# Kernel optimization log

Measured on AMD Instinct MI355X. Metric: run time of the kernel, lower is better.

The kernel has to match this reference:

```python
import jax, jax.numpy as jnp
import numpy as np


def setup_inputs() -> dict:
    key = jax.random.key(0)
    ks = jax.random.split(key, 7)
    B, C, L, A = 8, 1024, 2048, 128
    x = jax.random.normal(ks[0], (B, C, L), dtype=jnp.float32)
    Wk = jax.random.normal(ks[1], (A, C), dtype=jnp.float32) * (1.0 / np.sqrt(C))
    bk = jax.random.normal(ks[2], (A,), dtype=jnp.float32) * 0.01
    Wq = jax.random.normal(ks[3], (A, C), dtype=jnp.float32) * (1.0 / np.sqrt(C))
    bq = jax.random.normal(ks[4], (A,), dtype=jnp.float32) * 0.01
    Wp = jax.random.normal(ks[5], (C, C), dtype=jnp.float32) * (1.0 / np.sqrt(C))
    bp = jax.random.normal(ks[6], (C,), dtype=jnp.float32) * 0.01
    return {"x": x, "Wk": Wk, "bk": bk, "Wq": Wq, "bq": bq, "Wp": Wp, "bp": bp}


def reference(x, Wk, bk, Wq, bq, Wp, bp):
    # x: [B, C, L]; 1x1 Conv1d == pointwise linear over channel dim
    keys = jnp.einsum('bcl,ac->bal', x, Wk) + bk[None, :, None]      # [B, A, L]
    queries = jnp.einsum('bcl,ac->bal', x, Wq) + bq[None, :, None]   # [B, A, L]
    values = jnp.einsum('bal,bam->blm', keys, queries)               # keys^T @ queries -> [B, L, L]
    seqlen = x.shape[2]
    # NOTE: source uses seqlen ** 1 / 2 which is seqlen/2 due to Python precedence
    attn = jax.nn.softmax(values / (seqlen / 2.0), axis=-1)          # [B, L, L]
    out = jnp.einsum('bcl,blm->bcm', x, attn)                        # x @ attn -> [B, C, L]
    out = jnp.einsum('bcm,dc->bdm', out, Wp) + bp[None, :, None]     # output projection
    return out
```

## Files before the change

kernel.cpp:

```cpp
#include <hip/hip_runtime.h>
#include <hip/hip_bf16.h>

typedef __hip_bfloat16 bf16;
typedef __attribute__((ext_vector_type(8))) short bfrag8;
typedef __attribute__((ext_vector_type(8))) int intx8;
typedef __attribute__((ext_vector_type(4))) float floatx4;


__device__ __forceinline__ unsigned char f2fp8(float f) {
    f = fminf(fmaxf(f, -448.f), 448.f);
    return (unsigned char)(__builtin_amdgcn_cvt_pk_fp8_f32(f, f, 0, false) & 0xFF);
}

__device__ __forceinline__ void async_copy16(const void* g, void* lds) {
    __builtin_amdgcn_global_load_lds(
        (const __attribute__((address_space(1))) unsigned int*)g,
        (__attribute__((address_space(3))) unsigned int*)lds, 16, 0, 0);
}

template<int BIASMODE, int OUTKIND, bool EXPZ, bool MFAST>
__global__ __launch_bounds__(256)
void gemm128(const bf16* __restrict__ Ag, long sAb, int lda,
             const bf16* __restrict__ Bg, long sBb, int ldb,
             void* __restrict__ Cg, long sCb, int ldc,
             const float* __restrict__ scl, const float* __restrict__ b2,
             float* __restrict__ Zp, int K, int logfast)
{
    __shared__ unsigned short As[128 * 64];
    __shared__ unsigned short Bs[128 * 64];

    const int lin = blockIdx.x;
    const int bz  = lin & 7;
    const int s   = lin >> 3;
    const int msk = (1 << logfast) - 1;
    int mT, nT;
    if (MFAST) { mT = s & msk; nT = s >> logfast; }
    else       { nT = s & msk; mT = s >> logfast; }

    const bf16* A  = Ag + (size_t)bz * sAb + (size_t)mT * 128 * lda;
    const bf16* Bp = Bg + (size_t)bz * sBb + (size_t)nT * 128 * ldb;
    const int t = threadIdx.x, wave = t >> 6, lane = t & 63;
    const int qrow = lane & 15, quad = lane >> 4;
    const int wr = (wave >> 1) * 64, wc = (wave & 1) * 64;

    floatx4 acc[4][4] = {};

    for (int k0 = 0; k0 < K; k0 += 64) {
        #pragma unroll
        for (int j = 0; j < 4; ++j) {
            int c = j * 256 + t;
            int r = c >> 3, p = c & 7;
            int g = p ^ (r & 7);
            async_copy16(A + (size_t)r * lda + k0 + g * 8, &As[c * 8]);
        }
        #pragma unroll
        for (int j = 0; j < 4; ++j) {
            int c = j * 256 + t;
            int r = c >> 3, p = c & 7;
            int g = p ^ (r & 7);
            async_copy16(Bp + (size_t)r * ldb + k0 + g * 8, &Bs[c * 8]);
        }
        __syncthreads();

        #pragma unroll
        for (int ks = 0; ks < 2; ++ks) {
            bfrag8 af[4], bfv[4];
            #pragma unroll
            for (int mi = 0; mi < 4; ++mi) {
                int row = wr + mi * 16 + qrow;
                int ck  = ks * 4 + quad;
                af[mi] = *(const bfrag8*)&As[row * 64 + ((ck ^ (row & 7)) * 8)];
            }
            #pragma unroll
            for (int ni = 0; ni < 4; ++ni) {
                int row = wc + ni * 16 + qrow;
                int ck  = ks * 4 + quad;
                bfv[ni] = *(const bfrag8*)&Bs[row * 64 + ((ck ^ (row & 7)) * 8)];
            }
            #pragma unroll
            for (int mi = 0; mi < 4; ++mi)
                #pragma unroll
                for (int ni = 0; ni < 4; ++ni)
                    acc[mi][ni] = __builtin_amdgcn_mfma_f32_16x16x32_bf16(
                        af[mi], bfv[ni], acc[mi][ni], 0, 0, 0);
        }
        __syncthreads();
    }

    const int bmr = mT * 128 + wr, bnc = nT * 128 + wc;
    float zp[4] = {0.f, 0.f, 0.f, 0.f};
    #pragma unroll
    for (int mi = 0; mi < 4; ++mi) {
        #pragma unroll
        for (int ni = 0; ni < 4; ++ni) {
            int col = bnc + ni * 16 + qrow;
            #pragma unroll
            for (int r = 0; r < 4; ++r) {
                int row = bmr + mi * 16 + quad * 4 + r;
                float v = acc[mi][ni][r];
                if (EXPZ) { float e = __expf(v); zp[ni] += e; v = (e - 1.0f) * 4096.0f; }
                if (BIASMODE == 1) v = v * scl[col] + b2[col];
                if (BIASMODE == 2) v += scl[row];
                if (OUTKIND == 1)
                    ((float*)Cg + (size_t)bz * sCb)[(size_t)row * ldc + col] = v;
                else if (OUTKIND == 0)
                    ((bf16*)Cg + (size_t)bz * sCb)[(size_t)row * ldc + col] = __float2bfloat16(v);
                else
                    ((unsigned char*)Cg + (size_t)bz * sCb)[(size_t)row * ldc + col] = f2fp8(v);
            }
        }
    }
    if (EXPZ) {
        #pragma unroll
        for (int ni = 0; ni < 4; ++ni) {
            float tt = zp[ni];
            tt += __shfl_xor(tt, 16, 64);
            tt += __shfl_xor(tt, 32, 64);
            if (quad == 0)
                atomicAdd(&Zp[bz * 2048 + bnc + ni * 16 + qrow], tt);
        }
    }
}

__global__ __launch_bounds__(512, 2)
void gemm_s3(const bf16* __restrict__ Ag, long sAb, int lda,
             const bf16* __restrict__ Bg, long sBb, int ldb,
             unsigned char* __restrict__ Cg, long sCb, int ldc,
             float* __restrict__ Zp)
{
    __shared__ __align__(16) unsigned char smem[131072];

    const int lin = blockIdx.x;
    const int bz  = lin & 7;
    const int s0  = lin >> 3;
    const int nT  = s0 & 7, mT = s0 >> 3;

    const bf16* A  = Ag + (size_t)bz * sAb + (size_t)mT * 256 * lda;
    const bf16* Bp = Bg + (size_t)bz * sBb + (size_t)nT * 256 * ldb;
    const int t = threadIdx.x, wave = t >> 6, lane = t & 63;
    const int qrow = lane & 15, quad = lane >> 4;
    const int wm = (wave >> 2) * 128;
    const int wn = (wave & 3) * 64;

    unsigned char* As = smem;
    unsigned char* Bs = smem + 65536;

    #pragma unroll
    for (int j = 0; j < 8; ++j) {
        int c = j * 512 + t;
        int r = c >> 4, p = c & 15;
        int g = (p & 8) | ((p & 7) ^ (r & 7));
        async_copy16(A + (size_t)r * lda + g * 8, As + c * 16);
    }
    #pragma unroll
    for (int j = 0; j < 8; ++j) {
        int c = j * 512 + t;
        int r = c >> 4, p = c & 15;
        int g = (p & 8) | ((p & 7) ^ (r & 7));
        async_copy16(Bp + (size_t)r * ldb + g * 8, Bs + c * 16);
    }
    asm volatile("s_waitcnt vmcnt(0)" ::: "memory");
    __builtin_amdgcn_s_barrier();

    floatx4 acc[8][4] = {};
    #pragma unroll
    for (int ks = 0; ks < 4; ++ks) {
        const int ck = ks * 4 + quad;
        bfrag8 bfv[4];
        #pragma unroll
        for (int ni = 0; ni < 4; ++ni) {
            int row = wn + ni * 16 + qrow;
            int ph  = (ck & 8) | ((ck & 7) ^ (row & 7));
            bfv[ni] = *(const bfrag8*)&Bs[row * 256 + ph * 16];
        }
        #pragma unroll
        for (int mi = 0; mi < 8; ++mi) {
            int row = wm + mi * 16 + qrow;
            int ph  = (ck & 8) | ((ck & 7) ^ (row & 7));
            bfrag8 af = *(const bfrag8*)&As[row * 256 + ph * 16];
            #pragma unroll
            for (int ni = 0; ni < 4; ++ni)
                acc[mi][ni] = __builtin_amdgcn_mfma_f32_16x16x32_bf16(
                    af, bfv[ni], acc[mi][ni], 0, 0, 0);
        }
    }

    const int bmr = mT * 256 + wm, bnc = nT * 256 + wn;
    unsigned char* C8 = Cg + (size_t)bz * sCb;
    float zp[4] = {0.f, 0.f, 0.f, 0.f};
    #pragma unroll
    for (int mi = 0; mi < 8; ++mi) {
        #pragma unroll
        for (int ni = 0; ni < 4; ++ni) {
            int col = bnc + ni * 16 + qrow;
            #pragma unroll
            for (int r = 0; r < 4; ++r) {
                int row = bmr + mi * 16 + quad * 4 + r;
                float e = __expf(acc[mi][ni][r]);
                zp[ni] += e;
                C8[(size_t)row * ldc + col] = f2fp8((e - 1.0f) * 4096.0f);
            }
        }
    }
    #pragma unroll
    for (int ni = 0; ni < 4; ++ni) {
        float tt = zp[ni];
        tt += __shfl_xor(tt, 16, 64);
        tt += __shfl_xor(tt, 32, 64);
        if (quad == 0)
            atomicAdd(&Zp[bz * 2048 + bnc + ni * 16 + qrow], tt);
    }
}

template<int MODE, bool MFAST>
__global__ __launch_bounds__(512, 2)
void gemm_f8(const unsigned char* __restrict__ Ag, long sAb, int lda,
             const unsigned char* __restrict__ Bg, long sBb, int ldb,
             void* __restrict__ Cg, long sCb, int ldc,
             const float* __restrict__ rowb, float os, int K, int logfast)
{
    __shared__ __align__(16) unsigned char smem[131072];

    const int lin = blockIdx.x;
    const int bz  = lin & 7;
    const int s0  = lin >> 3;
    const int msk = (1 << logfast) - 1;
    int mT, nT;
    if (MFAST) { mT = s0 & msk; nT = s0 >> logfast; }
    else       { nT = s0 & msk; mT = s0 >> logfast; }

    const unsigned char* A  = Ag + (size_t)bz * sAb + (size_t)mT * 256 * lda;
    const unsigned char* Bp = Bg + (size_t)bz * sBb + (size_t)nT * 256 * ldb;
    const int t = threadIdx.x, wave = t >> 6, lane = t & 63;
    const int qrow = lane & 15, quad = lane >> 4;
    const int wm = (wave >> 2) * 128;
    const int wn = (wave & 3) * 64;

    floatx4 acc[8][4] = {};

    auto stage_part = [&](int kt, int slot, int part) {
        const int k0 = kt << 7;
        unsigned char* Ad = &smem[slot * 32768];
        unsigned char* Bd = &smem[65536 + slot * 32768];
        #pragma unroll
        for (int j = 0; j < 2; ++j) {
            int c = (part * 2 + j) * 512 + t;
            int r = c >> 3, p = c & 7, g = p ^ (r & 7);
            async_copy16(A + (size_t)r * lda + k0 + g * 16, Ad + c * 16);
        }
        #pragma unroll
        for (int j = 0; j < 2; ++j) {
            int c = (part * 2 + j) * 512 + t;
            int r = c >> 3, p = c & 7, g = p ^ (r & 7);
            async_copy16(Bp + (size_t)r * ldb + k0 + g * 16, Bd + c * 16);
        }
    };

    const int NT = K >> 7;
    stage_part(0, 0, 0);
    stage_part(0, 0, 1);

    for (int kt = 0; kt < NT; ++kt) {
        const int slot = kt & 1;
        const unsigned char* As = &smem[slot * 32768];
        const unsigned char* Bs = &smem[65536 + slot * 32768];

        asm volatile("s_waitcnt vmcnt(0)" ::: "memory");
        __builtin_amdgcn_sched_barrier(0);
        __builtin_amdgcn_s_barrier();
        __builtin_amdgcn_sched_barrier(0);

        intx8 bfr[4];
        #pragma unroll
        for (int ph = 0; ph < 4; ++ph) {
            if (ph == 0) {
                #pragma unroll
                for (int ni = 0; ni < 4; ++ni) {
                    int row = wn + ni * 16 + qrow, sw = row & 7;
                    union { intx8 v; uint4 q[2]; } u;
                    u.q[0] = *(const uint4*)&Bs[row * 128 + (((quad * 2    ) ^ sw) * 16)];
                    u.q[1] = *(const uint4*)&Bs[row * 128 + (((quad * 2 + 1) ^ sw) * 16)];
                    bfr[ni] = u.v;
                }
            }
            intx8 af0, af1;
            {
                int row = wm + (2 * ph) * 16 + qrow, sw = row & 7;
                union { intx8 v; uint4 q[2]; } u;
                u.q[0] = *(const uint4*)&As[row * 128 + (((quad * 2    ) ^ sw) * 16)];
                u.q[1] = *(const uint4*)&As[row * 128 + (((quad * 2 + 1) ^ sw) * 16)];
                af0 = u.v;
            }
            {
                int row = wm + (2 * ph + 1) * 16 + qrow, sw = row & 7;
                union { intx8 v; uint4 q[2]; } u;
                u.q[0] = *(const uint4*)&As[row * 128 + (((quad * 2    ) ^ sw) * 16)];
                u.q[1] = *(const uint4*)&As[row * 128 + (((quad * 2 + 1) ^ sw) * 16)];
                af1 = u.v;
            }
            if (ph < 2 && kt + 1 < NT) stage_part(kt + 1, slot ^ 1, ph);

            __builtin_amdgcn_sched_barrier(0);
            __builtin_amdgcn_s_barrier();
            asm volatile("s_waitcnt lgkmcnt(0)" ::: "memory");
            __builtin_amdgcn_sched_barrier(0);

            __builtin_amdgcn_s_setprio(1);
            #pragma unroll
            for (int ni = 0; ni < 4; ++ni)
                acc[2 * ph][ni] = __builtin_amdgcn_mfma_scale_f32_16x16x128_f8f6f4(
                    af0, bfr[ni], acc[2 * ph][ni], 0, 0, 0, 127, 0, 127);
            #pragma unroll
            for (int ni = 0; ni < 4; ++ni)
                acc[2 * ph + 1][ni] = __builtin_amdgcn_mfma_scale_f32_16x16x128_f8f6f4(
                    af1, bfr[ni], acc[2 * ph + 1][ni], 0, 0, 0, 127, 0, 127);
            __builtin_amdgcn_s_setprio(0);

            __builtin_amdgcn_sched_barrier(0);
            __builtin_amdgcn_s_barrier();
            __builtin_amdgcn_sched_barrier(0);
        }
    }

    const int bmr = mT * 256 + wm, bnc = nT * 256 + wn;
    #pragma unroll
    for (int mi = 0; mi < 8; ++mi) {
        int row0 = bmr + mi * 16 + quad * 4;
        float4 rb4;
        if (MODE == 2) rb4 = *(const float4*)&rowb[bz * 1024 + row0];
        #pragma unroll
        for (int ni = 0; ni < 4; ++ni) {
            int col = bnc + ni * 16 + qrow;
            floatx4 a = acc[mi][ni];
            if (MODE == 2) {
                float* Co = (float*)Cg + (size_t)bz * sCb;
                Co[(size_t)(row0 + 0) * ldc + col] = a[0] * os + rb4.x;
                Co[(size_t)(row0 + 1) * ldc + col] = a[1] * os + rb4.y;
                Co[(size_t)(row0 + 2) * ldc + col] = a[2] * os + rb4.z;
                Co[(size_t)(row0 + 3) * ldc + col] = a[3] * os + rb4.w;
            } else {
                unsigned char* C8 = (unsigned char*)Cg + (size_t)bz * sCb;
                #pragma unroll
                for (int r = 0; r < 4; ++r)
                    C8[(size_t)(row0 + r) * ldc + col] = f2fp8(a[r] * os);
            }
        }
    }
}

__global__ __launch_bounds__(256)
void conv_w(const float* __restrict__ Wk, const float* __restrict__ Wq,
            const float* __restrict__ Wp, bf16* __restrict__ Wkqb,
            unsigned char* __restrict__ Wp8)
{
    int i = blockIdx.x * 256 + threadIdx.x;
    if (i < 32768) {
        const float* src = (i < 16384) ? Wk : Wq;
        int off = (i < 16384) ? i : i - 16384;
        bf16* dst = Wkqb + (size_t)((i < 16384) ? 0 : 131072);
        const float4* sp = (const float4*)src + (size_t)off * 2;
        float4 a = sp[0], b = sp[1];
        union { uint4 u; unsigned short h[8]; } o;
        union { bf16 h; unsigned short u; } cv;
        cv.h = __float2bfloat16(a.x); o.h[0] = cv.u;
        cv.h = __float2bfloat16(a.y); o.h[1] = cv.u;
        cv.h = __float2bfloat16(a.z); o.h[2] = cv.u;
        cv.h = __float2bfloat16(a.w); o.h[3] = cv.u;
        cv.h = __float2bfloat16(b.x); o.h[4] = cv.u;
        cv.h = __float2bfloat16(b.y); o.h[5] = cv.u;
        cv.h = __float2bfloat16(b.z); o.h[6] = cv.u;
        cv.h = __float2bfloat16(b.w); o.h[7] = cv.u;
        ((uint4*)dst)[off] = o.u;
    } else {
        int off = i - 32768;
        const float4* sp = (const float4*)Wp + (size_t)off * 2;
        float4 a = sp[0], b = sp[1];
        unsigned char o[8];
        o[0] = f2fp8(a.x * 2048.f); o[1] = f2fp8(a.y * 2048.f);
        o[2] = f2fp8(a.z * 2048.f); o[3] = f2fp8(a.w * 2048.f);
        o[4] = f2fp8(b.x * 2048.f); o[5] = f2fp8(b.y * 2048.f);
        o[6] = f2fp8(b.z * 2048.f); o[7] = f2fp8(b.w * 2048.f);
        uint2 w;
        w.x = (unsigned int)o[0] | ((unsigned int)o[1] << 8) | ((unsigned int)o[2] << 16) | ((unsigned int)o[3] << 24);
        w.y = (unsigned int)o[4] | ((unsigned int)o[5] << 8) | ((unsigned int)o[6] << 16) | ((unsigned int)o[7] << 24);
        ((uint2*)Wp8)[off] = w;
    }
}

__global__ __launch_bounds__(256)
void conv_x(const float* __restrict__ x, bf16* __restrict__ xt)
{
    const int b = blockIdx.z;
    const int l0 = blockIdx.x * 64, c0 = blockIdx.y * 64;
    const float* xp = x + (size_t)b * 1024 * 2048;
    bf16* xtp = xt + (size_t)b * 2048 * 1024;
    __shared__ unsigned short tile[64][65];
    const int t = threadIdx.x, tr = t >> 4, tc4 = (t & 15) * 4;
    union { bf16 h; unsigned short u; } cv;
    #pragma unroll
    for (int i = 0; i < 4; ++i) {
        int r = i * 16 + tr;
        float4 v = *(const float4*)(xp + (size_t)(c0 + r) * 2048 + l0 + tc4);
        cv.h = __float2bfloat16(v.x); tile[r][tc4]     = cv.u;
        cv.h = __float2bfloat16(v.y); tile[r][tc4 + 1] = cv.u;
        cv.h = __float2bfloat16(v.z); tile[r][tc4 + 2] = cv.u;
        cv.h = __float2bfloat16(v.w); tile[r][tc4 + 3] = cv.u;
    }
    __syncthreads();
    #pragma unroll
    for (int i = 0; i < 4; ++i) {
        int lr = i * 16 + tr;
        union { uint2 u; unsigned short h[4]; } o;
        #pragma unroll
        for (int j = 0; j < 4; ++j) o.h[j] = tile[tc4 + j][lr];
        *(uint2*)(xtp + (size_t)(l0 + lr) * 1024 + c0 + tc4) = o.u;
    }
}

__global__ void prep_bias(const float* __restrict__ bk, const float* __restrict__ bq,
                          float* __restrict__ scl, float* __restrict__ b2, float kscale)
{
    int t = threadIdx.x;
    float s = (t < 128) ? kscale : 1.0f;
    scl[t] = s;
    b2[t] = ((t < 128) ? bk[t] : bq[t - 128]) * s;
}

__global__ __launch_bounds__(256)
void normx(const float* __restrict__ x, const float* __restrict__ Z,
           unsigned char* __restrict__ xs, float* __restrict__ colsum)
{
    const int bc = blockIdx.x;
    const int b  = bc >> 10;
    const int t  = threadIdx.x;
    const float* xp = x + (size_t)bc * 2048 + t * 8;
    const float* zp = Z + b * 2048 + t * 8;
    float4 a = ((const float4*)xp)[0], c4 = ((const float4*)xp)[1];
    float4 z0 = ((const float4*)zp)[0], z1 = ((const float4*)zp)[1];
    float v[8];
    v[0] = a.x  / fmaxf(z0.x, 1e-10f); v[1] = a.y / fmaxf(z0.y, 1e-10f);
    v[2] = a.z  / fmaxf(z0.z, 1e-10f); v[3] = a.w / fmaxf(z0.w, 1e-10f);
    v[4] = c4.x / fmaxf(z1.x, 1e-10f); v[5] = c4.y / fmaxf(z1.y, 1e-10f);
    v[6] = c4.z / fmaxf(z1.z, 1e-10f); v[7] = c4.w / fmaxf(z1.w, 1e-10f);
    float s = 0.f;
    unsigned char o[8];
    #pragma unroll
    for (int j = 0; j < 8; ++j) { s += v[j]; o[j] = f2fp8(v[j] * 65536.f); }
    uint2 w;
    w.x = (unsigned int)o[0] | ((unsigned int)o[1] << 8) | ((unsigned int)o[2] << 16) | ((unsigned int)o[3] << 24);
    w.y = (unsigned int)o[4] | ((unsigned int)o[5] << 8) | ((unsigned int)o[6] << 16) | ((unsigned int)o[7] << 24);
    ((uint2*)(xs + (size_t)bc * 2048))[t] = w;
    #pragma unroll
    for (int off = 32; off >= 1; off >>= 1) s += __shfl_xor(s, off, 64);
    __shared__ float red[4];
    if ((t & 63) == 0) red[t >> 6] = s;
    __syncthreads();
    if (t == 0) colsum[bc] = red[0] + red[1] + red[2] + red[3];
}

__global__ __launch_bounds__(256)
void basek(const float* __restrict__ Wp, const float* __restrict__ colsum,
           const float* __restrict__ bp, float* __restrict__ base)
{
    const int d = blockIdx.x, t = threadIdx.x;
    float4 w = *(const float4*)(Wp + (size_t)d * 1024 + t * 4);
    float pb[8];
    #pragma unroll
    for (int b = 0; b < 8; ++b) {
        float4 cs = *(const float4*)(colsum + b * 1024 + t * 4);
        pb[b] = w.x * cs.x + w.y * cs.y + w.z * cs.z + w.w * cs.w;
    }
    __shared__ float red[8][4];
    #pragma unroll
    for (int b = 0; b < 8; ++b) {
        float s = pb[b];
        #pragma unroll
        for (int off = 32; off >= 1; off >>= 1) s += __shfl_xor(s, off, 64);
        if ((t & 63) == 0) red[b][t >> 6] = s;
    }
    __syncthreads();
    if (t < 8) base[t * 1024 + d] = bp[d] + red[t][0] + red[t][1] + red[t][2] + red[t][3];
}

extern "C" void kernel_launch(void* const* d_in, const int* in_sizes, int n_in,
                              void* d_out, int out_size, void* d_ws, size_t ws_size,
                              hipStream_t stream)
{
    const float* x  = (const float*)d_in[0];
    const float* Wk = (const float*)d_in[1];
    const float* bk = (const float*)d_in[2];
    const float* Wq = (const float*)d_in[3];
    const float* bq = (const float*)d_in[4];
    const float* Wp = (const float*)d_in[5];
    const float* bp = (const float*)d_in[6];
    float* out = (float*)d_out;

    const float kscale = 2.0f / 2048.0f;

    bf16* xt   = (bf16*)d_ws;
    bf16* KQt  = xt + (size_t)8 * 2048 * 1024;
    bf16* Wkqb = KQt + (size_t)8 * 2048 * 256;
    unsigned char* Wp8 = (unsigned char*)(Wkqb + (size_t)256 * 1024);
    unsigned char* St8 = Wp8 + (size_t)1048576;
    unsigned char* xs8 = St8 + (size_t)8 * 2048 * 2048;
    float* Z      = (float*)(xs8 + (size_t)8 * 1024 * 2048);
    float* colsum = Z + 8 * 2048;
    float* base   = colsum + 8 * 1024;
    float* scl    = base + 8 * 1024;
    float* b2     = scl + 256;
    unsigned char* Dlt = (unsigned char*)xt;

    dim3 blk(256, 1, 1);
    dim3 blk512(512, 1, 1);

    prep_bias<<<dim3(1), blk, 0, stream>>>(bk, bq, scl, b2, kscale);
    conv_w<<<dim3(640), blk, 0, stream>>>(Wk, Wq, Wp, Wkqb, Wp8);
    conv_x<<<dim3(32, 16, 8), blk, 0, stream>>>(x, xt);

    gemm128<1, 0, false, false><<<dim3(8 * 16 * 2), blk, 0, stream>>>(
        xt, 2048L * 1024, 1024,  Wkqb, 0, 1024,
        KQt, 2048L * 256, 256,  scl, b2, nullptr, 1024, 1);

    hipMemsetAsync(Z, 0, (size_t)8 * 2048 * sizeof(float), stream);

    gemm_s3<<<dim3(8 * 8 * 8), blk512, 0, stream>>>(
        KQt + 128, 2048L * 256, 256,  KQt, 2048L * 256, 256,
        St8, 2048L * 2048, 2048,  Z);

    normx<<<dim3(8 * 1024), blk, 0, stream>>>(x, Z, xs8, colsum);
    basek<<<dim3(1024), blk, 0, stream>>>(Wp, colsum, bp, base);

    gemm_f8<0, false><<<dim3(8 * 8 * 4), blk512, 0, stream>>>(
        St8, 2048L * 2048, 2048,  xs8, 1024L * 2048, 2048,
        Dlt, 2048L * 1024, 1024,  nullptr, 0.0009765625f, 2048, 2);

    gemm_f8<2, true><<<dim3(8 * 4 * 8), blk512, 0, stream>>>(
        Wp8, 0, 1024,  Dlt, 2048L * 1024, 1024,
        out, 1024L * 2048, 2048,  base, 1.862645149230957e-9f, 1024, 2);
}
```

Before: 261.8 us.

## Fuse x transpose/bf16 conversion into K/Q projection GEMM and merge setup kernels

Removes the separate conv_x transpose pass by having the K/Q projection GEMM load fp32 x tiles directly into LDS and convert them to bf16 while building MFMA fragments. It also folds prep_bias and the Z memset into the weight-conversion kernel, which cuts the launch count. The GEMM now uses 64x256 tiles with 256 blocks. Doing the conversion in the inner loop adds strided LDS reads and VALU work, and 256 blocks may underfill the GPU.

Result: faster. 245.4 us (-6.3%).

```diff
diff --git a/kernel.cpp b/kernel.cpp
--- a/kernel.cpp
+++ b/kernel.cpp
@@ -18,106 +18,84 @@
         (__attribute__((address_space(3))) unsigned int*)lds, 16, 0, 0);
 }
 
-template<int BIASMODE, int OUTKIND, bool EXPZ, bool MFAST>
 __global__ __launch_bounds__(256)
-void gemm128(const bf16* __restrict__ Ag, long sAb, int lda,
-             const bf16* __restrict__ Bg, long sBb, int ldb,
-             void* __restrict__ Cg, long sCb, int ldc,
-             const float* __restrict__ scl, const float* __restrict__ b2,
-             float* __restrict__ Zp, int K, int logfast)
-{
-    __shared__ unsigned short As[128 * 64];
-    __shared__ unsigned short Bs[128 * 64];
+void gemm12(const float* __restrict__ xg, const bf16* __restrict__ Wkqb,
+            bf16* __restrict__ KQt, const float* __restrict__ scl,
+            const float* __restrict__ b2)
+{
+    __shared__ __align__(16) float Xs[64 * 64];
+    __shared__ __align__(16) unsigned short Ws[256 * 64];
 
     const int lin = blockIdx.x;
     const int bz  = lin & 7;
-    const int s   = lin >> 3;
-    const int msk = (1 << logfast) - 1;
-    int mT, nT;
-    if (MFAST) { mT = s & msk; nT = s >> logfast; }
-    else       { nT = s & msk; mT = s >> logfast; }
-
-    const bf16* A  = Ag + (size_t)bz * sAb + (size_t)mT * 128 * lda;
-    const bf16* Bp = Bg + (size_t)bz * sBb + (size_t)nT * 128 * ldb;
+    const int mT  = lin >> 3;
+    const int l0  = mT * 64;
+    const float* xp = xg + (size_t)bz * 1024 * 2048;
+
     const int t = threadIdx.x, wave = t >> 6, lane = t & 63;
     const int qrow = lane & 15, quad = lane >> 4;
-    const int wr = (wave >> 1) * 64, wc = (wave & 1) * 64;
-
-    floatx4 acc[4][4] = {};
-
-    for (int k0 = 0; k0 < K; k0 += 64) {
+    const int wr = (wave >> 1) * 32, wc = (wave & 1) * 128;
+
+    floatx4 acc[2][8] = {};
+
+    for (int k0 = 0; k0 < 1024; k0 += 64) {
         #pragma unroll
         for (int j = 0; j < 4; ++j) {
-            int c = j * 256 + t;
-            int r = c >> 3, p = c & 7;
-            int g = p ^ (r & 7);
-            async_copy16(A + (size_t)r * lda + k0 + g * 8, &As[c * 8]);
-        }
-        #pragma unroll
-        for (int j = 0; j < 4; ++j) {
-            int c = j * 256 + t;
-            int r = c >> 3, p = c & 7;
-            int g = p ^ (r & 7);
-            async_copy16(Bp + (size_t)r * ldb + k0 + g * 8, &Bs[c * 8]);
-        }
+            int ci = j * 256 + t;
+            int r = ci >> 4, li = (ci & 15) * 4;
+            async_copy16(xp + (size_t)(k0 + r) * 2048 + l0 + li, &Xs[ci * 4]);
+        }
+        #pragma unroll
+        for (int j = 0; j < 8; ++j) {
+            int ci = j * 256 + t;
+            int r = ci >> 3, p = ci & 7, g = p ^ (r & 7);
+            async_copy16(Wkqb + (size_t)r * 1024 + k0 + g * 8, &Ws[ci * 8]);
+        }
+        asm volatile("s_waitcnt vmcnt(0)" ::: "memory");
         __syncthreads();
 
         #pragma unroll
         for (int ks = 0; ks < 2; ++ks) {
-            bfrag8 af[4], bfv[4];
-            #pragma unroll
-            for (int mi = 0; mi < 4; ++mi) {
-                int row = wr + mi * 16 + qrow;
-                int ck  = ks * 4 + quad;
-                af[mi] = *(const bfrag8*)&As[row * 64 + ((ck ^ (row & 7)) * 8)];
-            }
-            #pragma unroll
-            for (int ni = 0; ni < 4; ++ni) {
+            const int ck = ks * 4 + quad;
+            bfrag8 bfv[8];
+            #pragma unroll
+            for (int ni = 0; ni < 8; ++ni) {
                 int row = wc + ni * 16 + qrow;
-                int ck  = ks * 4 + quad;
-                bfv[ni] = *(const bfrag8*)&Bs[row * 64 + ((ck ^ (row & 7)) * 8)];
-            }
-            #pragma unroll
-            for (int mi = 0; mi < 4; ++mi)
+                bfv[ni] = *(const bfrag8*)&Ws[row * 64 + ((ck ^ (row & 7)) * 8)];
+            }
+            #pragma unroll
+            for (int mi = 0; mi < 2; ++mi) {
+                int l = wr + mi * 16 + qrow;
+                union { bfrag8 v; unsigned short h[8]; } af;
+                union { bf16 bh; unsigned short u; } cv;
                 #pragma unroll
-                for (int ni = 0; ni < 4; ++ni)
+                for (int j = 0; j < 8; ++j) {
+                    float f = Xs[(ck * 8 + j) * 64 + l];
+                    cv.bh = __float2bfloat16(f);
+                    af.h[j] = cv.u;
+                }
+                #pragma unroll
+                for (int ni = 0; ni < 8; ++ni)
                     acc[mi][ni] = __builtin_amdgcn_mfma_f32_16x16x32_bf16(
-                        af[mi], bfv[ni], acc[mi][ni], 0, 0, 0);
+                        af.v, bfv[ni], acc[mi][ni], 0, 0, 0);
+            }
         }
         __syncthreads();
     }
 
-    const int bmr = mT * 128 + wr, bnc = nT * 128 + wc;
-    float zp[4] = {0.f, 0.f, 0.f, 0.f};
-    #pragma unroll
-    for (int mi = 0; mi < 4; ++mi) {
-        #pragma unroll
-        for (int ni = 0; ni < 4; ++ni) {
+    const int bmr = l0 + wr, bnc = wc;
+    bf16* Cp = KQt + (size_t)bz * 2048 * 256;
+    #pragma unroll
+    for (int mi = 0; mi < 2; ++mi) {
+        #pragma unroll
+        for (int ni = 0; ni < 8; ++ni) {
             int col = bnc + ni * 16 + qrow;
+            float sc = scl[col], bb = b2[col];
             #pragma unroll
             for (int r = 0; r < 4; ++r) {
                 int row = bmr + mi * 16 + quad * 4 + r;
-                float v = acc[mi][ni][r];
-                if (EXPZ) { float e = __expf(v); zp[ni] += e; v = (e - 1.0f) * 4096.0f; }
-                if (BIASMODE == 1) v = v * scl[col] + b2[col];
-                if (BIASMODE == 2) v += scl[row];
-                if (OUTKIND == 1)
-                    ((float*)Cg + (size_t)bz * sCb)[(size_t)row * ldc + col] = v;
-                else if (OUTKIND == 0)
-                    ((bf16*)Cg + (size_t)bz * sCb)[(size_t)row * ldc + col] = __float2bfloat16(v);
-                else
-                    ((unsigned char*)Cg + (size_t)bz * sCb)[(size_t)row * ldc + col] = f2fp8(v);
-            }
-        }
-    }
-    if (EXPZ) {
-        #pragma unroll
-        for (int ni = 0; ni < 4; ++ni) {
-            float tt = zp[ni];
-            tt += __shfl_xor(tt, 16, 64);
-            tt += __shfl_xor(tt, 32, 64);
-            if (quad == 0)
-                atomicAdd(&Zp[bz * 2048 + bnc + ni * 16 + qrow], tt);
+                Cp[(size_t)row * 256 + col] = __float2bfloat16(acc[mi][ni][r] * sc + bb);
+            }
         }
     }
 }
@@ -349,11 +327,29 @@
 }
 
 __global__ __launch_bounds__(256)
-void conv_w(const float* __restrict__ Wk, const float* __restrict__ Wq,
-            const float* __restrict__ Wp, bf16* __restrict__ Wkqb,
-            unsigned char* __restrict__ Wp8)
-{
-    int i = blockIdx.x * 256 + threadIdx.x;
+void conv_wz(const float* __restrict__ Wk, const float* __restrict__ Wq,
+             const float* __restrict__ Wp, bf16* __restrict__ Wkqb,
+             unsigned char* __restrict__ Wp8,
+             const float* __restrict__ bk, const float* __restrict__ bq,
+             float* __restrict__ scl, float* __restrict__ b2,
+             float* __restrict__ Z, float kscale)
+{
+    const int blk = blockIdx.x;
+    const int t   = threadIdx.x;
+    if (blk == 640) {
+        float s = (t < 128) ? kscale : 1.0f;
+        scl[t] = s;
+        b2[t] = ((t < 128) ? bk[t] : bq[t - 128]) * s;
+        return;
+    }
+    if (blk >= 641) {
+        float4 z = make_float4(0.f, 0.f, 0.f, 0.f);
+        float* zp = Z + (size_t)(blk - 641) * 4096 + t * 16;
+        #pragma unroll
+        for (int j = 0; j < 4; ++j) *(float4*)(zp + j * 4) = z;
+        return;
+    }
+    int i = blk * 256 + t;
     if (i < 32768) {
         const float* src = (i < 16384) ? Wk : Wq;
         int off = (i < 16384) ? i : i - 16384;
@@ -388,45 +384,6 @@
 }
 
 __global__ __launch_bounds__(256)
-void conv_x(const float* __restrict__ x, bf16* __restrict__ xt)
-{
-    const int b = blockIdx.z;
-    const int l0 = blockIdx.x * 64, c0 = blockIdx.y * 64;
-    const float* xp = x + (size_t)b * 1024 * 2048;
-    bf16* xtp = xt + (size_t)b * 2048 * 1024;
-    __shared__ unsigned short tile[64][65];
-    const int t = threadIdx.x, tr = t >> 4, tc4 = (t & 15) * 4;
-    union { bf16 h; unsigned short u; } cv;
-    #pragma unroll
-    for (int i = 0; i < 4; ++i) {
-        int r = i * 16 + tr;
-        float4 v = *(const float4*)(xp + (size_t)(c0 + r) * 2048 + l0 + tc4);
-        cv.h = __float2bfloat16(v.x); tile[r][tc4]     = cv.u;
-        cv.h = __float2bfloat16(v.y); tile[r][tc4 + 1] = cv.u;
-        cv.h = __float2bfloat16(v.z); tile[r][tc4 + 2] = cv.u;
-        cv.h = __float2bfloat16(v.w); tile[r][tc4 + 3] = cv.u;
-    }
-    __syncthreads();
-    #pragma unroll
-    for (int i = 0; i < 4; ++i) {
-        int lr = i * 16 + tr;
-        union { uint2 u; unsigned short h[4]; } o;
-        #pragma unroll
-        for (int j = 0; j < 4; ++j) o.h[j] = tile[tc4 + j][lr];
-        *(uint2*)(xtp + (size_t)(l0 + lr) * 1024 + c0 + tc4) = o.u;
-    }
-}
-
-__global__ void prep_bias(const float* __restrict__ bk, const float* __restrict__ bq,
-                          float* __restrict__ scl, float* __restrict__ b2, float kscale)
-{
-    int t = threadIdx.x;
-    float s = (t < 128) ? kscale : 1.0f;
-    scl[t] = s;
-    b2[t] = ((t < 128) ? bk[t] : bq[t - 128]) * s;
-}
-
-__global__ __launch_bounds__(256)
 void normx(const float* __restrict__ x, const float* __restrict__ Z,
            unsigned char* __restrict__ xs, float* __restrict__ colsum)
 {
@@ -508,20 +465,15 @@
     float* base   = colsum + 8 * 1024;
     float* scl    = base + 8 * 1024;
     float* b2     = scl + 256;
-    unsigned char* Dlt = (unsigned char*)xt;
+    unsigned char* Dlt = (unsigned char*)d_ws;
 
     dim3 blk(256, 1, 1);
     dim3 blk512(512, 1, 1);
 
-    prep_bias<<<dim3(1), blk, 0, stream>>>(bk, bq, scl, b2, kscale);
-    conv_w<<<dim3(640), blk, 0, stream>>>(Wk, Wq, Wp, Wkqb, Wp8);
-    conv_x<<<dim3(32, 16, 8), blk, 0, stream>>>(x, xt);
-
-    gemm128<1, 0, false, false><<<dim3(8 * 16 * 2), blk, 0, stream>>>(
-        xt, 2048L * 1024, 1024,  Wkqb, 0, 1024,
-        KQt, 2048L * 256, 256,  scl, b2, nullptr, 1024, 1);
-
-    hipMemsetAsync(Z, 0, (size_t)8 * 2048 * sizeof(float), stream);
+    conv_wz<<<dim3(645), blk, 0, stream>>>(Wk, Wq, Wp, Wkqb, Wp8,
+                                           bk, bq, scl, b2, Z, kscale);
+
+    gemm12<<<dim3(256), blk, 0, stream>>>(x, Wkqb, KQt, scl, b2);
 
     gemm_s3<<<dim3(8 * 8 * 8), blk512, 0, stream>>>(
         KQt + 128, 2048L * 256, 256,  KQt, 2048L * 256, 256,
```
